# Kernel tuning notes

Hardware: AMD Instinct MI355X
Metric: run time of the kernel (lower is better)

## Reference

```python
import jax, jax.numpy as jnp
import numpy as np

N_NODES = 50000
N_EDGES = 800000
DIM = 64
N_ETYPES = 4
N_STEPS = 5


def setup_inputs() -> dict:
    key = jax.random.key(0)
    ks = jax.random.split(key, 10)
    feat = jax.random.normal(ks[0], (N_NODES, DIM), dtype=jnp.float32)
    src = jax.random.randint(ks[1], (N_EDGES,), 0, N_NODES, dtype=jnp.int32)
    dst = jax.random.randint(ks[2], (N_EDGES,), 0, N_NODES, dtype=jnp.int32)
    etypes = jax.random.randint(ks[3], (N_EDGES,), 0, N_ETYPES, dtype=jnp.int32)
    # per-edge-type Linear weights, xavier_normal with relu gain, zero bias
    gain = float(np.sqrt(2.0))
    std = gain * float(np.sqrt(2.0 / (DIM + DIM)))
    W = jax.random.normal(ks[4], (N_ETYPES, DIM, DIM), dtype=jnp.float32) * std  # [T, out, in]
    b = jnp.zeros((N_ETYPES, DIM), dtype=jnp.float32)
    # GRUCell params (torch layout: [3*dim, dim], gates order r,z,n), uniform(-1/sqrt(dim), 1/sqrt(dim))
    bound = 1.0 / float(np.sqrt(DIM))
    w_ih = jax.random.uniform(ks[5], (3 * DIM, DIM), minval=-bound, maxval=bound, dtype=jnp.float32)
    w_hh = jax.random.uniform(ks[6], (3 * DIM, DIM), minval=-bound, maxval=bound, dtype=jnp.float32)
    b_ih = jax.random.uniform(ks[7], (3 * DIM,), minval=-bound, maxval=bound, dtype=jnp.float32)
    b_hh = jax.random.uniform(ks[8], (3 * DIM,), minval=-bound, maxval=bound, dtype=jnp.float32)
    return {"feat": feat, "W": W, "b": b, "w_ih": w_ih, "w_hh": w_hh,
            "b_ih": b_ih, "b_hh": b_hh, "src": src, "dst": dst, "etypes": etypes}


def _gru_cell(a, h, w_ih, w_hh, b_ih, b_hh):
    gi = a @ w_ih.T + b_ih  # [N, 3*D]
    gh = h @ w_hh.T + b_hh
    i_r, i_z, i_n = jnp.split(gi, 3, axis=-1)
    h_r, h_z, h_n = jnp.split(gh, 3, axis=-1)
    r = jax.nn.sigmoid(i_r + h_r)
    z = jax.nn.sigmoid(i_z + h_z)
    n = jnp.tanh(i_n + r * h_n)
    return (1.0 - z) * n + z * h


def reference(feat, W, b, w_ih, w_hh, b_ih, b_hh, src, dst, etypes):
    n_nodes = feat.shape[0]
    h = feat
    for _ in range(N_STEPS):
        # apply every etype linear to all nodes: [N, T, D]
        h_all = jnp.einsum('nd,ted->nte', h, W) + b
        # per-edge message selects src node under its edge type: [E, D]
        m = h_all[src, etypes]
        # scatter-sum to destination nodes: [N, D]
        a = jax.ops.segment_sum(m, dst, num_segments=n_nodes)
        h = _gru_cell(a, h, w_ih, w_hh, b_ih, b_hh)
    return h
```

## Files before the change

kernel.cpp:

```cpp
#include <hip/hip_runtime.h>
#include <hip/hip_bf16.h>
#include <cstdint>

#define DIM 64
#define TD 256
#define NSTEPS 5
#define GLD 194
#define HS  68
#define MAXDEG 64

typedef __attribute__((ext_vector_type(8))) short short8v;
typedef __attribute__((ext_vector_type(4))) float f32x4;
typedef __attribute__((ext_vector_type(8))) _Float16 half8v;

__device__ __forceinline__ float sigmoidf_(float x){ return 1.0f/(1.0f+expf(-x)); }

__device__ __forceinline__ unsigned short f2bf(float x){
  unsigned u = __builtin_bit_cast(unsigned, x);
  return (unsigned short)((u + 0x7FFFu + ((u>>16)&1u)) >> 16);
}
__device__ __forceinline__ float bf2f(unsigned short b){
  unsigned u = ((unsigned)b)<<16;
  return __builtin_bit_cast(float, u);
}

__device__ __forceinline__ void splitbf8(const float* __restrict__ p,
                                         short8v& hi, short8v& lo){
  float4 x0 = *(const float4*)p;
  float4 x1 = *(const float4*)(p+4);
  float xs[8] = {x0.x,x0.y,x0.z,x0.w,x1.x,x1.y,x1.z,x1.w};
#pragma unroll
  for(int i=0;i<8;i++){
    unsigned short hb = f2bf(xs[i]);
    float rem = xs[i] - bf2f(hb);
    hi[i] = (short)hb;
    lo[i] = (short)f2bf(rem);
  }
}

__global__ __launch_bounds__(256) void k_pack(const float* __restrict__ src,
    short* __restrict__ ph, short* __restrict__ pl, int ncoltiles, int mode){
  int idx = blockIdx.x*256 + threadIdx.x;
  int total = ncoltiles*1024;
  if (idx >= total) return;
  int e = idx & 7, lane = (idx>>3)&63, kc = (idx>>9)&1, ct = idx>>10;
  int col = ct*16 + (lane&15);
  int k = kc*32 + (lane>>4)*8 + e;
  float v;
  if (mode==0){ int t = col>>6, eo = col&63; v = src[(size_t)(t*64+eo)*64 + k]; }
  else        { v = src[(size_t)col*64 + k]; }
  unsigned short hb = f2bf(v);
  float rem = v - bf2f(hb);
  ph[idx] = (short)hb;
  pl[idx] = (short)f2bf(rem);
}

__global__ __launch_bounds__(256) void k_transform_mfma(
    const float* __restrict__ h, const short* __restrict__ pth,
    const short* __restrict__ ptl, const float* __restrict__ b,
    _Float16* __restrict__ h_all, int n_nodes){
  const int wave = threadIdx.x >> 6, lane = threadIdx.x & 63;
  const int n0 = blockIdx.x * 16;
  if (n0 >= n_nodes) return;
  const int arow = n0 + (lane & 15);
  const int kb = (lane >> 4) * 8;
  short8v ah0,al0,ah1,al1;
  splitbf8(h + (size_t)arow*DIM + kb,      ah0, al0);
  splitbf8(h + (size_t)arow*DIM + 32 + kb, ah1, al1);
  const int crow = n0 + (lane >> 4) * 4;
  const int cc = lane & 15;
#pragma unroll
  for (int i = 0; i < 4; ++i){
    int ct = wave*4 + i;
    const short8v bh0 = *(const short8v*)(pth + ((size_t)(ct*2+0)*64 + lane)*8);
    const short8v bh1 = *(const short8v*)(pth + ((size_t)(ct*2+1)*64 + lane)*8);
    const short8v bl0 = *(const short8v*)(ptl + ((size_t)(ct*2+0)*64 + lane)*8);
    const short8v bl1 = *(const short8v*)(ptl + ((size_t)(ct*2+1)*64 + lane)*8);
    float bias = b[ct*16 + cc];
    f32x4 acc = {bias,bias,bias,bias};
    acc = __builtin_amdgcn_mfma_f32_16x16x32_bf16(ah0, bh0, acc, 0,0,0);
    acc = __builtin_amdgcn_mfma_f32_16x16x32_bf16(ah1, bh1, acc, 0,0,0);
    acc = __builtin_amdgcn_mfma_f32_16x16x32_bf16(al0, bh0, acc, 0,0,0);
    acc = __builtin_amdgcn_mfma_f32_16x16x32_bf16(al1, bh1, acc, 0,0,0);
    acc = __builtin_amdgcn_mfma_f32_16x16x32_bf16(ah0, bl0, acc, 0,0,0);
    acc = __builtin_amdgcn_mfma_f32_16x16x32_bf16(ah1, bl1, acc, 0,0,0);
#pragma unroll
    for (int q=0;q<4;q++)
      h_all[(size_t)(crow + q)*TD + ct*16 + cc] = (_Float16)acc[q];
  }
}

__global__ __launch_bounds__(256) void k_scatter_ell(
    const int* __restrict__ src, const int* __restrict__ dst,
    const int* __restrict__ et, int* __restrict__ deg,
    int* __restrict__ ell, int n_edges) {
  int e = blockIdx.x * 256 + threadIdx.x;
  if (e >= n_edges) return;
  int d0 = dst[e];
  int rank = atomicAdd(&deg[d0], 1);
  if (rank < MAXDEG)
    ell[(size_t)d0 * MAXDEG + rank] = (src[e] << 2) | et[e];
}

__global__ __launch_bounds__(256) void k_step(
    const _Float16* __restrict__ h_in, _Float16* __restrict__ h_out,
    const int* __restrict__ ell, const int* __restrict__ deg,
    float* __restrict__ h,
    const short* __restrict__ pih_h, const short* __restrict__ pih_l,
    const short* __restrict__ phh_h, const short* __restrict__ phh_l,
    const float* __restrict__ b_ih, const float* __restrict__ b_hh,
    const short* __restrict__ pth, const short* __restrict__ ptl,
    const float* __restrict__ bb,
    int n_nodes, int do_transform){
  __shared__ float atile[16][HS];
  __shared__ float gbuf[2][16][GLD];
  __shared__ float hnew[16][HS];
  const int tid = threadIdx.x;
  const int wave = tid >> 6, lane = tid & 63;
  const int n0 = blockIdx.x * 16;
  if (n0 >= n_nodes) return;

  {
    int j = tid >> 4;
    int q = tid & 15;
    int eslot = q >> 3;
    int dimg = q & 7;
    int node = n0 + j;
    int dg = min(deg[node], MAXDEG);
    const size_t ebase = (size_t)node * MAXDEG;
    float acc[8] = {0,0,0,0,0,0,0,0};
    int i = eslot;
    for (; i + 2 < dg; i += 4) {
      int p0 = ell[ebase + i];
      int p1 = ell[ebase + i + 2];
      half8v v0 = *(const half8v*)(h_in + (size_t)(p0>>2)*TD + (p0&3)*DIM + dimg*8);
      half8v v1 = *(const half8v*)(h_in + (size_t)(p1>>2)*TD + (p1&3)*DIM + dimg*8);
#pragma unroll
      for (int k=0;k<8;k++) acc[k] += (float)v0[k] + (float)v1[k];
    }
    for (; i < dg; i += 2) {
      int p0 = ell[ebase + i];
      half8v v0 = *(const half8v*)(h_in + (size_t)(p0>>2)*TD + (p0&3)*DIM + dimg*8);
#pragma unroll
      for (int k=0;k<8;k++) acc[k] += (float)v0[k];
    }
#pragma unroll
    for (int k=0;k<8;k++) acc[k] += __shfl_xor(acc[k], 8);
    if (eslot == 0) {
#pragma unroll
      for (int k=0;k<8;k++) atile[j][dimg*8+k] = acc[k];
    }
  }
  __syncthreads();

  const bool is_h = wave >= 2;
  const short* __restrict__ pbh = is_h ? phh_h : pih_h;
  const short* __restrict__ pbl = is_h ? phh_l : pih_l;
  const float* __restrict__ bv  = is_h ? b_hh : b_ih;
  float* outb = &gbuf[is_h ? 1 : 0][0][0];

  const int kb = (lane >> 4) * 8;
  short8v ah0,al0,ah1,al1;
  if (is_h) {
    const float* xp = h + (size_t)(n0 + (lane & 15))*DIM;
    splitbf8(xp + kb,      ah0, al0);
    splitbf8(xp + 32 + kb, ah1, al1);
  } else {
    const float* xp = &atile[lane & 15][0];
    splitbf8(xp + kb,      ah0, al0);
    splitbf8(xp + 32 + kb, ah1, al1);
  }

  const int ct0 = (wave & 1) * 6;
  const int rr = (lane >> 4) * 4;
  const int cc = lane & 15;
#pragma unroll
  for (int i = 0; i < 6; ++i){
    int ct = ct0 + i;
    const short8v bh0 = *(const short8v*)(pbh + ((size_t)(ct*2+0)*64 + lane)*8);
    const short8v bh1 = *(const short8v*)(pbh + ((size_t)(ct*2+1)*64 + lane)*8);
    const short8v bl0 = *(const short8v*)(pbl + ((size_t)(ct*2+0)*64 + lane)*8);
    const short8v bl1 = *(const short8v*)(pbl + ((size_t)(ct*2+1)*64 + lane)*8);
    float bias = bv[ct*16 + cc];
    f32x4 acc = {bias,bias,bias,bias};
    acc = __builtin_amdgcn_mfma_f32_16x16x32_bf16(ah0, bh0, acc, 0,0,0);
    acc = __builtin_amdgcn_mfma_f32_16x16x32_bf16(ah1, bh1, acc, 0,0,0);
    acc = __builtin_amdgcn_mfma_f32_16x16x32_bf16(al0, bh0, acc, 0,0,0);
    acc = __builtin_amdgcn_mfma_f32_16x16x32_bf16(al1, bh1, acc, 0,0,0);
    acc = __builtin_amdgcn_mfma_f32_16x16x32_bf16(ah0, bl0, acc, 0,0,0);
    acc = __builtin_amdgcn_mfma_f32_16x16x32_bf16(ah1, bl1, acc, 0,0,0);
#pragma unroll
    for (int q=0;q<4;q++)
      outb[(rr+q)*GLD + ct*16 + cc] = acc[q];
  }
  __syncthreads();

#pragma unroll
  for (int it=0; it<4; ++it){
    int t = it*256 + tid;
    int j = t >> 6, d = t & 63;
    float r  = sigmoidf_(gbuf[0][j][d]      + gbuf[1][j][d]);
    float z  = sigmoidf_(gbuf[0][j][64+d]   + gbuf[1][j][64+d]);
    float nv = tanhf    (gbuf[0][j][128+d]  + r*gbuf[1][j][128+d]);
    size_t off = (size_t)(n0+j)*DIM + d;
    float ho = h[off];
    float hn = (1.0f - z)*nv + z*ho;
    h[off] = hn;
    hnew[j][d] = hn;
  }
  if (!do_transform) return;
  __syncthreads();

  short8v th0,tl0,th1,tl1;
  splitbf8(&hnew[lane & 15][kb],      th0, tl0);
  splitbf8(&hnew[lane & 15][32 + kb], th1, tl1);
  const int crow = n0 + (lane >> 4) * 4;
#pragma unroll
  for (int i = 0; i < 4; ++i){
    int ct = wave*4 + i;
    const short8v bh0 = *(const short8v*)(pth + ((size_t)(ct*2+0)*64 + lane)*8);
    const short8v bh1 = *(const short8v*)(pth + ((size_t)(ct*2+1)*64 + lane)*8);
    const short8v bl0 = *(const short8v*)(ptl + ((size_t)(ct*2+0)*64 + lane)*8);
    const short8v bl1 = *(const short8v*)(ptl + ((size_t)(ct*2+1)*64 + lane)*8);
    float bias = bb[ct*16 + cc];
    f32x4 acc = {bias,bias,bias,bias};
    acc = __builtin_amdgcn_mfma_f32_16x16x32_bf16(th0, bh0, acc, 0,0,0);
    acc = __builtin_amdgcn_mfma_f32_16x16x32_bf16(th1, bh1, acc, 0,0,0);
    acc = __builtin_amdgcn_mfma_f32_16x16x32_bf16(tl0, bh0, acc, 0,0,0);
    acc = __builtin_amdgcn_mfma_f32_16x16x32_bf16(tl1, bh1, acc, 0,0,0);
    acc = __builtin_amdgcn_mfma_f32_16x16x32_bf16(th0, bl0, acc, 0,0,0);
    acc = __builtin_amdgcn_mfma_f32_16x16x32_bf16(th1, bl1, acc, 0,0,0);
#pragma unroll
    for (int q=0;q<4;q++)
      h_out[(size_t)(crow + q)*TD + ct*16 + cc] = (_Float16)acc[q];
  }
}

extern "C" void kernel_launch(void* const* d_in, const int* in_sizes, int n_in,
                              void* d_out, int out_size, void* d_ws, size_t ws_size,
                              hipStream_t stream) {
  const float* feat = (const float*)d_in[0];
  const float* W    = (const float*)d_in[1];
  const float* b    = (const float*)d_in[2];
  const float* w_ih = (const float*)d_in[3];
  const float* w_hh = (const float*)d_in[4];
  const float* b_ih = (const float*)d_in[5];
  const float* b_hh = (const float*)d_in[6];
  const int* src = (const int*)d_in[7];
  const int* dst = (const int*)d_in[8];
  const int* et  = (const int*)d_in[9];

  const int n_nodes = in_sizes[0] / DIM;
  const int n_edges = in_sizes[7];

  float* h = (float*)d_out;
  char* ws = (char*)d_ws;
  _Float16* hall0 = (_Float16*)ws;  ws += (size_t)n_nodes * TD * sizeof(_Float16);
  _Float16* hall1 = (_Float16*)ws;  ws += (size_t)n_nodes * TD * sizeof(_Float16);
  int* ell     = (int*)ws;      ws += (size_t)n_nodes * MAXDEG * sizeof(int);
  int* deg     = (int*)ws;      ws += (size_t)n_nodes * sizeof(int);
  short* pt_h  = (short*)ws;    ws += 16384 * sizeof(short);
  short* pt_l  = (short*)ws;    ws += 16384 * sizeof(short);
  short* pih_h = (short*)ws;    ws += 12288 * sizeof(short);
  short* pih_l = (short*)ws;    ws += 12288 * sizeof(short);
  short* phh_h = (short*)ws;    ws += 12288 * sizeof(short);
  short* phh_l = (short*)ws;    ws += 12288 * sizeof(short);

  hipMemcpyAsync(h, feat, (size_t)n_nodes * DIM * sizeof(float),
                 hipMemcpyDeviceToDevice, stream);

  k_pack<<<64, 256, 0, stream>>>(W,    pt_h,  pt_l,  16, 0);
  k_pack<<<48, 256, 0, stream>>>(w_ih, pih_h, pih_l, 12, 1);
  k_pack<<<48, 256, 0, stream>>>(w_hh, phh_h, phh_l, 12, 1);

  const int nblk_edges = (n_edges + 255) / 256;
  hipMemsetAsync(deg, 0, (size_t)n_nodes * sizeof(int), stream);
  k_scatter_ell<<<nblk_edges, 256, 0, stream>>>(src, dst, et, deg, ell, n_edges);

  const int rtiles = (n_nodes + 15) / 16;

  k_transform_mfma<<<rtiles, 256, 0, stream>>>(h, pt_h, pt_l, b, hall0, n_nodes);
  for (int s = 0; s < NSTEPS; ++s) {
    const _Float16* hin = (s & 1) ? hall1 : hall0;
    _Float16* hout      = (s & 1) ? hall0 : hall1;
    k_step<<<rtiles, 256, 0, stream>>>(hin, hout, ell, deg, h,
                                       pih_h, pih_l, phh_h, phh_l, b_ih, b_hh,
                                       pt_h, pt_l, b, n_nodes,
                                       (s < NSTEPS - 1) ? 1 : 0);
  }
}
```

Baseline: 322.1 us.

## Stage ELL rows in LDS, unroll gather by four, store gates as fp16

The kernel now cooperatively loads each block's 16 ELL adjacency rows into shared memory before the neighbor gather. The gather loop is unrolled to four loads in flight per thread. The GRU gate buffer is stored as fp16 instead of fp32 and shares LDS with the staged ELL rows, which shrinks the shared-memory footprint to allow more resident blocks. In exchange there is an extra barrier, ELL rows are loaded in full even for low-degree nodes, and storing gate pre-activations in fp16 loses precision.

```diff
diff --git a/kernel.cpp b/kernel.cpp
--- a/kernel.cpp
+++ b/kernel.cpp
@@ -5,8 +5,8 @@
 #define DIM 64
 #define TD 256
 #define NSTEPS 5
-#define GLD 194
 #define HS  68
+#define GLDH 194
 #define MAXDEG 64
 
 typedef __attribute__((ext_vector_type(8))) short short8v;
@@ -112,13 +112,23 @@
     const short* __restrict__ pth, const short* __restrict__ ptl,
     const float* __restrict__ bb,
     int n_nodes, int do_transform){
-  __shared__ float atile[16][HS];
-  __shared__ float gbuf[2][16][GLD];
-  __shared__ float hnew[16][HS];
+  __shared__ __align__(16) char smem[4352 + 12416];
+  float (*atile)[HS]      = (float(*)[HS])smem;
+  float (*hnew)[HS]       = (float(*)[HS])smem;
+  int   (*ells)[MAXDEG]   = (int(*)[MAXDEG])(smem + 4352);
+  _Float16* gbuf          = (_Float16*)(smem + 4352);
+
   const int tid = threadIdx.x;
   const int wave = tid >> 6, lane = tid & 63;
   const int n0 = blockIdx.x * 16;
   if (n0 >= n_nodes) return;
+
+  {
+    int j = tid >> 4, c4 = (tid & 15) * 4;
+    int4 v = *(const int4*)(ell + (size_t)(n0 + j) * MAXDEG + c4);
+    *(int4*)&ells[j][c4] = v;
+  }
+  __syncthreads();
 
   {
     int j = tid >> 4;
@@ -127,19 +137,20 @@
     int dimg = q & 7;
     int node = n0 + j;
     int dg = min(deg[node], MAXDEG);
-    const size_t ebase = (size_t)node * MAXDEG;
     float acc[8] = {0,0,0,0,0,0,0,0};
     int i = eslot;
-    for (; i + 2 < dg; i += 4) {
-      int p0 = ell[ebase + i];
-      int p1 = ell[ebase + i + 2];
+    for (; i + 6 < dg; i += 8) {
+      int p0 = ells[j][i], p1 = ells[j][i+2], p2 = ells[j][i+4], p3 = ells[j][i+6];
       half8v v0 = *(const half8v*)(h_in + (size_t)(p0>>2)*TD + (p0&3)*DIM + dimg*8);
       half8v v1 = *(const half8v*)(h_in + (size_t)(p1>>2)*TD + (p1&3)*DIM + dimg*8);
-#pragma unroll
-      for (int k=0;k<8;k++) acc[k] += (float)v0[k] + (float)v1[k];
+      half8v v2 = *(const half8v*)(h_in + (size_t)(p2>>2)*TD + (p2&3)*DIM + dimg*8);
+      half8v v3 = *(const half8v*)(h_in + (size_t)(p3>>2)*TD + (p3&3)*DIM + dimg*8);
+#pragma unroll
+      for (int k=0;k<8;k++)
+        acc[k] += ((float)v0[k] + (float)v1[k]) + ((float)v2[k] + (float)v3[k]);
     }
     for (; i < dg; i += 2) {
-      int p0 = ell[ebase + i];
+      int p0 = ells[j][i];
       half8v v0 = *(const half8v*)(h_in + (size_t)(p0>>2)*TD + (p0&3)*DIM + dimg*8);
 #pragma unroll
       for (int k=0;k<8;k++) acc[k] += (float)v0[k];
@@ -157,7 +168,7 @@
   const short* __restrict__ pbh = is_h ? phh_h : pih_h;
   const short* __restrict__ pbl = is_h ? phh_l : pih_l;
   const float* __restrict__ bv  = is_h ? b_hh : b_ih;
-  float* outb = &gbuf[is_h ? 1 : 0][0][0];
+  _Float16* outb = gbuf + (is_h ? 16*GLDH : 0);
 
   const int kb = (lane >> 4) * 8;
   short8v ah0,al0,ah1,al1;
@@ -191,7 +202,7 @@
     acc = __builtin_amdgcn_mfma_f32_16x16x32_bf16(ah1, bl1, acc, 0,0,0);
 #pragma unroll
     for (int q=0;q<4;q++)
-      outb[(rr+q)*GLD + ct*16 + cc] = acc[q];
+      outb[(rr+q)*GLDH + ct*16 + cc] = (_Float16)acc[q];
   }
   __syncthreads();
 
@@ -199,9 +210,15 @@
   for (int it=0; it<4; ++it){
     int t = it*256 + tid;
     int j = t >> 6, d = t & 63;
-    float r  = sigmoidf_(gbuf[0][j][d]      + gbuf[1][j][d]);
-    float z  = sigmoidf_(gbuf[0][j][64+d]   + gbuf[1][j][64+d]);
-    float nv = tanhf    (gbuf[0][j][128+d]  + r*gbuf[1][j][128+d]);
+    float gir = (float)gbuf[j*GLDH + d];
+    float giz = (float)gbuf[j*GLDH + 64 + d];
+    float gin = (float)gbuf[j*GLDH + 128 + d];
+    float ghr = (float)gbuf[16*GLDH + j*GLDH + d];
+    float ghz = (float)gbuf[16*GLDH + j*GLDH + 64 + d];
+    float ghn = (float)gbuf[16*GLDH + j*GLDH + 128 + d];
+    float r  = sigmoidf_(gir + ghr);
+    float z  = sigmoidf_(giz + ghz);
+    float nv = tanhf    (gin + r*ghn);
     size_t off = (size_t)(n0+j)*DIM + d;
     float ho = h[off];
     float hn = (1.0f - z)*nv + z*ho;
```

Result: faster. 308.8 us (-4.1%).
